# Kernel optimization log

Hardware: AMD Instinct MI355X
Metric: run time of the kernel (lower is better)

The kernel has to match this reference:

```python
import jax, jax.numpy as jnp
import numpy as np
import math

HEADS = 32
DIM_HEAD = 64
DM = HEADS * DIM_HEAD  # 2048
B, S = 2, 1024
BITS = 3
N_LEVELS = 2 ** BITS
N_GROUPS = (DIM_HEAD + 2) // 3  # 22
PAD = (3 - DIM_HEAD % 3) % 3    # 2
EPS_NORM = 1e-8
EPS_RMS = 1e-6


def _rotors_to_matrices(r):
    # r: (G,4) unit rotors [s, b12, b13, b23] -> (G,3,3) rotation matrices
    s, p, q, rr = r[:, 0], r[:, 1], r[:, 2], r[:, 3]
    s2, p2, q2, r2 = s * s, p * p, q * q, rr * rr
    M = np.zeros((r.shape[0], 3, 3), dtype=np.float32)
    M[:, 0, 0] = s2 - p2 - q2 + r2
    M[:, 0, 1] = 2 * s * p - 2 * q * rr
    M[:, 0, 2] = 2 * s * q + 2 * p * rr
    M[:, 1, 0] = -2 * s * p - 2 * q * rr
    M[:, 1, 1] = s2 - p2 + q2 - r2
    M[:, 1, 2] = 2 * s * rr - 2 * p * q
    M[:, 2, 0] = -2 * s * q + 2 * p * rr
    M[:, 2, 1] = -2 * s * rr - 2 * p * q
    M[:, 2, 2] = s2 + p2 - q2 - r2
    return M


def _make_compressor(seed):
    rng = np.random.default_rng(seed)
    rot = rng.standard_normal((N_GROUPS, 4)).astype(np.float32)
    rot /= np.linalg.norm(rot, axis=-1, keepdims=True)
    M = _rotors_to_matrices(rot)
    sigma = 1.0 / math.sqrt(DIM_HEAD)  # Lloyd-Max for N(0, 1/d)
    C = np.linspace(-3 * sigma, 3 * sigma, N_LEVELS, dtype=np.float32)
    return jnp.asarray(M), jnp.asarray(np.ascontiguousarray(M.transpose(0, 2, 1))), jnp.asarray(C)


def setup_inputs() -> dict:
    key = jax.random.key(0)
    ks = jax.random.split(key, 8)
    x = jax.random.normal(ks[0], (B, S, DM), dtype=jnp.float32)
    w_scale = 0.02
    Wq = jax.random.normal(ks[1], (DM, DM), dtype=jnp.float32) * w_scale
    Wk = jax.random.normal(ks[2], (DM, DM), dtype=jnp.float32) * w_scale
    Wv = jax.random.normal(ks[3], (DM, DM), dtype=jnp.float32) * w_scale
    Wo = jax.random.normal(ks[4], (DM, DM), dtype=jnp.float32) * w_scale
    qn_w = jnp.ones((DM,), dtype=jnp.float32)
    kn_w = jnp.ones((DM,), dtype=jnp.float32)
    Mk, Mtk, Ck = _make_compressor(42)
    Mv, Mtv, Cv = _make_compressor(4200)
    return {"x": x, "Wq": Wq, "Wk": Wk, "Wv": Wv, "Wo": Wo,
            "qn_w": qn_w, "kn_w": kn_w,
            "Mk": Mk, "Mtk": Mtk, "Ck": Ck,
            "Mv": Mv, "Mtv": Mtv, "Cv": Cv}


def _rmsnorm(x, w):
    return x * jax.lax.rsqrt(jnp.mean(x * x, axis=-1, keepdims=True) + EPS_RMS) * w


def _quant_roundtrip(h, M, Mt, C):
    """RotorQuant compress+decompress. h: (B,H,S,Dh) -> (B,H,S,Dh)."""
    norms = jnp.maximum(jnp.linalg.norm(h, axis=-1, keepdims=True), EPS_NORM)
    xu = h / norms
    xu = jnp.pad(xu, ((0, 0), (0, 0), (0, 0), (0, PAD)))
    g = xu.reshape(h.shape[0], h.shape[1], h.shape[2], N_GROUPS, 3)
    rot = jnp.einsum('bhsgi,gij->bhsgj', g, M)
    flat = rot.reshape(h.shape[0], h.shape[1], h.shape[2], N_GROUPS * 3)
    # nearest-centroid quantization (uint8 indices in original)
    idx = jnp.argmin(jnp.abs(flat[..., None] - C), axis=-1)
    deq = C[idx]
    g2 = deq.reshape(h.shape[0], h.shape[1], h.shape[2], N_GROUPS, 3)
    der = jnp.einsum('bhsgi,gij->bhsgj', g2, Mt)
    out = der.reshape(h.shape[0], h.shape[1], h.shape[2], N_GROUPS * 3)[..., :DIM_HEAD]
    return out * norms


def reference(x, Wq, Wk, Wv, Wo, qn_w, kn_w, Mk, Mtk, Ck, Mv, Mtv, Cv):
    b, s, _ = x.shape
    v = x @ Wv
    q = _rmsnorm(x @ Wq, qn_w)
    k = _rmsnorm(x @ Wk, kn_w)
    # split heads -> (B,H,S,Dh)
    qh = q.reshape(b, s, HEADS, DIM_HEAD).transpose(0, 2, 1, 3)
    kh = k.reshape(b, s, HEADS, DIM_HEAD).transpose(0, 2, 1, 3)
    vh = v.reshape(b, s, HEADS, DIM_HEAD).transpose(0, 2, 1, 3)
    # per-head rotor quantization roundtrip of K and V
    kh = _quant_roundtrip(kh, Mk, Mtk, Ck)
    vh = _quant_roundtrip(vh, Mv, Mtv, Cv)
    # scaled dot-product attention
    scores = jnp.einsum('bhqd,bhkd->bhqk', qh, kh) / math.sqrt(DIM_HEAD)
    probs = jax.nn.softmax(scores, axis=-1)
    o = jnp.einsum('bhqk,bhkd->bhqd', probs, vh)
    o = o.transpose(0, 2, 1, 3).reshape(b, s, DM)
    return o @ Wo
```

## Files before the change

kernel.cpp:

```cpp
#include <hip/hip_runtime.h>
#include <hip/hip_bf16.h>
#include <math.h>

#define HEADS 32
#define DIM_HEAD 64
#define DM 2048
#define BATCH 2
#define SEQ 1024
#define NROWS (BATCH * SEQ)
#define NVEC (NROWS * HEADS)
#define N_GROUPS 22
#define N_LEVELS 8
#define EPS_NORM 1e-8f
#define EPS_RMS 1e-6f

typedef float f32x4 __attribute__((ext_vector_type(4)));
typedef __bf16 bf16x8 __attribute__((ext_vector_type(8)));
typedef unsigned short u16x8 __attribute__((ext_vector_type(8)));
typedef unsigned short u16x4 __attribute__((ext_vector_type(4)));

__device__ __forceinline__ unsigned short f2bf(float x) {
  union { float f; unsigned u; } v; v.f = x;
  unsigned r = v.u + 0x7fffu + ((v.u >> 16) & 1u);
  return (unsigned short)(r >> 16);
}
__device__ __forceinline__ float bf2f(unsigned short h) {
  union { unsigned u; float f; } v; v.u = ((unsigned)h) << 16;
  return v.f;
}
__device__ __forceinline__ bf16x8 ldfrag(const unsigned short* p) {
  return __builtin_bit_cast(bf16x8, *(const u16x8*)p);
}
#define MFMA16(a, b, c) __builtin_amdgcn_mfma_f32_16x16x32_bf16((a), (b), (c), 0, 0, 0)

__device__ __forceinline__ void stage16(const unsigned short* g, unsigned short* lds) {
  __builtin_amdgcn_global_load_lds(
      (const __attribute__((address_space(1))) unsigned int*)g,
      (__attribute__((address_space(3))) unsigned int*)lds, 16, 0, 0);
}

#define WAITV(N) asm volatile("s_waitcnt vmcnt(" #N ")" ::: "memory")
#define WAITL0() asm volatile("s_waitcnt lgkmcnt(0)" ::: "memory")
#define SBARM()  asm volatile("s_barrier" ::: "memory")
#define SFENCE() __builtin_amdgcn_sched_barrier(0)

__global__ __launch_bounds__(256) void split_convert_kernel(
    const float* __restrict__ X, unsigned short* __restrict__ hi,
    unsigned short* __restrict__ lo, int n8) {
  const int i = blockIdx.x * 256 + threadIdx.x;
  if (i >= n8) return;
  const float4 a = ((const float4*)X)[2 * i];
  const float4 b = ((const float4*)X)[2 * i + 1];
  const float v[8] = {a.x, a.y, a.z, a.w, b.x, b.y, b.z, b.w};
  u16x8 h, l;
#pragma unroll
  for (int j = 0; j < 8; ++j) {
    const unsigned short hh = f2bf(v[j]);
    h[j] = hh;
    l[j] = f2bf(v[j] - bf2f(hh));
  }
  ((u16x8*)hi)[i] = h;
  if (lo) ((u16x8*)lo)[i] = l;
}

__global__ __launch_bounds__(256) void transpose_split_batch_kernel(
    const float* __restrict__ W0, const float* __restrict__ W1,
    const float* __restrict__ W2, const float* __restrict__ W3,
    unsigned short* __restrict__ T0h, unsigned short* __restrict__ T1h,
    unsigned short* __restrict__ T1l, unsigned short* __restrict__ T2h,
    unsigned short* __restrict__ T2l, unsigned short* __restrict__ T3h) {
  const int z = blockIdx.z;
  const float* W = (z == 0) ? W0 : (z == 1) ? W1 : (z == 2) ? W2 : W3;
  unsigned short* Th = (z == 0) ? T0h : (z == 1) ? T1h : (z == 2) ? T2h : T3h;
  unsigned short* Tl = (z == 1) ? T1l : (z == 2) ? T2l : nullptr;

  __shared__ float S[64][65];
  const int t = threadIdx.x;
  const int tk = blockIdx.y * 64, tm = blockIdx.x * 64;
  {
    const int r = t >> 2, cs = (t & 3) * 16;
    const float* src = W + (size_t)(tk + r) * DM + tm + cs;
#pragma unroll
    for (int j = 0; j < 16; j += 4) {
      float4 v = *(const float4*)(src + j);
      S[r][cs + j] = v.x; S[r][cs + j + 1] = v.y;
      S[r][cs + j + 2] = v.z; S[r][cs + j + 3] = v.w;
    }
  }
  __syncthreads();
  const int m = t >> 2, ks = (t & 3) * 16;
  u16x8 h0, h1, l0, l1;
#pragma unroll
  for (int j = 0; j < 8; ++j) {
    const float v = S[ks + j][m];
    const unsigned short hh = f2bf(v);
    h0[j] = hh; l0[j] = f2bf(v - bf2f(hh));
  }
#pragma unroll
  for (int j = 0; j < 8; ++j) {
    const float v = S[ks + 8 + j][m];
    const unsigned short hh = f2bf(v);
    h1[j] = hh; l1[j] = f2bf(v - bf2f(hh));
  }
  const size_t o = (size_t)(tm + m) * DM + tk + ks;
  *(u16x8*)&Th[o] = h0; *(u16x8*)&Th[o + 8] = h1;
  if (Tl) { *(u16x8*)&Tl[o] = l0; *(u16x8*)&Tl[o + 8] = l1; }
}

__global__ __launch_bounds__(512, 2) void gemm_plain8(
    const unsigned short* __restrict__ A, const unsigned short* __restrict__ B,
    float* __restrict__ C, int ntiles) {
  __shared__ unsigned short L[2][2][128 * 64];
  const int t = threadIdx.x, lane = t & 63, w = t >> 6;
  const int wr = w >> 2, wc = w & 3;
  const int gm0 = blockIdx.y * 128;
  const int gn0 = blockIdx.x * 128;
  const int z = blockIdx.z;
  const int k0 = z * (ntiles << 6);
  const int chunk = (lane & 7) ^ (lane >> 3);

  auto stg = [&](const unsigned short* g, int row0, int kt, unsigned short* dst) {
#pragma unroll
    for (int it = 0; it < 2; ++it) {
      const int r = (w << 4) + (it << 3) + (lane >> 3);
      stage16(g + (size_t)(row0 + r) * DM + kt + chunk * 8,
              dst + ((w << 4) + (it << 3)) * 64);
    }
  };

  f32x4 acc[4][2] = {};

  stg(A, gm0, k0, L[0][0]);
  stg(B, gn0, k0, L[0][1]);

  for (int tt = 0; tt < ntiles; ++tt) {
    const int c = tt & 1, n = c ^ 1;
    const bool pf = (tt + 1 < ntiles);
    if (pf) {
      const int ktn = k0 + ((tt + 1) << 6);
      stg(A, gm0, ktn, L[n][0]);
      stg(B, gn0, ktn, L[n][1]);
      WAITV(4);
    } else {
      WAITV(0);
    }
    SBARM(); SFENCE();
    const unsigned short* cA = L[c][0];
    const unsigned short* cB = L[c][1];
    bf16x8 fa[4][2], fb[2][2];
#pragma unroll
    for (int ks = 0; ks < 2; ++ks) {
      const int ch = ks * 4 + (lane >> 4);
#pragma unroll
      for (int i = 0; i < 4; ++i) {
        const int row = wr * 64 + i * 16 + (lane & 15);
        fa[i][ks] = ldfrag(&cA[row * 64 + ((ch ^ (row & 7)) << 3)]);
      }
#pragma unroll
      for (int j = 0; j < 2; ++j) {
        const int row = wc * 32 + j * 16 + (lane & 15);
        fb[j][ks] = ldfrag(&cB[row * 64 + ((ch ^ (row & 7)) << 3)]);
      }
    }
    WAITL0();
    __builtin_amdgcn_s_setprio(1);
#pragma unroll
    for (int i = 0; i < 4; ++i)
#pragma unroll
      for (int j = 0; j < 2; ++j)
#pragma unroll
        for (int ks = 0; ks < 2; ++ks)
          acc[i][j] = MFMA16(fa[i][ks], fb[j][ks], acc[i][j]);
    __builtin_amdgcn_s_setprio(0);
    SFENCE(); SBARM();
  }

  float* Cz = C + (size_t)z * NROWS * DM;
#pragma unroll
  for (int i = 0; i < 4; ++i) {
    const int row = gm0 + wr * 64 + i * 16 + ((lane >> 4) << 2);
#pragma unroll
    for (int j = 0; j < 2; ++j) {
      const int col = gn0 + wc * 32 + j * 16 + (lane & 15);
#pragma unroll
      for (int r = 0; r < 4; ++r)
        Cz[(size_t)(row + r) * DM + col] = acc[i][j][r];
    }
  }
}

__global__ __launch_bounds__(512, 2) void gemm_kv_split8(
    const unsigned short* __restrict__ Ah, const unsigned short* __restrict__ Al,
    const unsigned short* __restrict__ Bh, const unsigned short* __restrict__ Bl,
    float* __restrict__ kout, float* __restrict__ vout) {
  __shared__ unsigned short L[2][4][128 * 64];
  const int t = threadIdx.x, lane = t & 63, w = t >> 6;
  const int wr = w >> 2, wc = w & 3;
  const int gm0 = blockIdx.y * 128;
  const int nAbs = 2048 + blockIdx.x * 128;
  const int seg = nAbs >> 11;
  const int gn0 = nAbs & 2047;
  const int chunk = (lane & 7) ^ (lane >> 3);

  auto stg = [&](const unsigned short* g, int row0, int kt, unsigned short* dst) {
#pragma unroll
    for (int it = 0; it < 2; ++it) {
      const int r = (w << 4) + (it << 3) + (lane >> 3);
      stage16(g + (size_t)(row0 + r) * DM + kt + chunk * 8,
              dst + ((w << 4) + (it << 3)) * 64);
    }
  };

  f32x4 acc[4][2] = {};

  auto group = [&](const unsigned short* arrA, const unsigned short* arrB) {
    bf16x8 fa[4][2], fb[2][2];
#pragma unroll
    for (int ks = 0; ks < 2; ++ks) {
      const int ch = ks * 4 + (lane >> 4);
#pragma unroll
      for (int i = 0; i < 4; ++i) {
        const int row = wr * 64 + i * 16 + (lane & 15);
        fa[i][ks] = ldfrag(&arrA[row * 64 + ((ch ^ (row & 7)) << 3)]);
      }
#pragma unroll
      for (int j = 0; j < 2; ++j) {
        const int row = wc * 32 + j * 16 + (lane & 15);
        fb[j][ks] = ldfrag(&arrB[row * 64 + ((ch ^ (row & 7)) << 3)]);
      }
    }
    WAITL0();
    __builtin_amdgcn_s_setprio(1);
#pragma unroll
    for (int i = 0; i < 4; ++i)
#pragma unroll
      for (int j = 0; j < 2; ++j)
#pragma unroll
        for (int ks = 0; ks < 2; ++ks)
          acc[i][j] = MFMA16(fa[i][ks], fb[j][ks], acc[i][j]);
    __builtin_amdgcn_s_setprio(0);
  };

  stg(Ah, gm0, 0, L[0][0]);
  stg(Bh, nAbs, 0, L[0][1]);
  stg(Bl, nAbs, 0, L[0][2]);
  stg(Al, gm0, 0, L[0][3]);

  for (int tt = 0; tt < 32; ++tt) {
    const int c = tt & 1, n = c ^ 1;
    const bool pf = (tt + 1 < 32);
    const int ktn = (tt + 1) << 6;

    if (pf) { stg(Ah, gm0, ktn, L[n][0]); stg(Bh, nAbs, ktn, L[n][1]); WAITV(8); }
    else WAITV(4);
    SBARM(); SFENCE();
    group(L[c][0], L[c][1]);
    SFENCE(); SBARM();

    if (pf) { stg(Bl, nAbs, ktn, L[n][2]); WAITV(8); }
    else WAITV(2);
    SBARM(); SFENCE();
    group(L[c][0], L[c][2]);
    SFENCE(); SBARM();

    if (pf) { stg(Al, gm0, ktn, L[n][3]); WAITV(8); }
    else WAITV(0);
    SBARM(); SFENCE();
    group(L[c][3], L[c][1]);
    SFENCE(); SBARM();
  }

  float* C = (seg == 1) ? kout : vout;
#pragma unroll
  for (int i = 0; i < 4; ++i) {
    const int row = gm0 + wr * 64 + i * 16 + ((lane >> 4) << 2);
#pragma unroll
    for (int j = 0; j < 2; ++j) {
      const int col = gn0 + wc * 32 + j * 16 + (lane & 15);
#pragma unroll
      for (int r = 0; r < 4; ++r)
        C[(size_t)(row + r) * DM + col] = acc[i][j][r];
    }
  }
}

__global__ __launch_bounds__(256) void add2_f4_kernel(
    const float* __restrict__ a, const float* __restrict__ b,
    float* __restrict__ o, int n4) {
  const int i = blockIdx.x * 256 + threadIdx.x;
  if (i >= n4) return;
  const float4 x = ((const float4*)a)[i];
  const float4 y = ((const float4*)b)[i];
  ((float4*)o)[i] = make_float4(x.x + y.x, x.y + y.y, x.z + y.z, x.w + y.w);
}

__device__ __forceinline__ float wave_sum(float x) {
#pragma unroll
  for (int o = 32; o > 0; o >>= 1) x += __shfl_xor(x, o, 64);
  return x;
}

__global__ __launch_bounds__(256) void rmsnorm_kernel(
    float* __restrict__ y, const float* __restrict__ w) {
  __shared__ float rbuf[4];
  const int row = blockIdx.x;
  float* p = y + (size_t)row * DM;
  const int t = threadIdx.x;
  const int wave = t >> 6, lane = t & 63;

  float ss = 0.f;
#pragma unroll
  for (int c = t; c < DM; c += 256) { float v = p[c]; ss += v * v; }
  ss = wave_sum(ss);
  if (lane == 0) rbuf[wave] = ss;
  __syncthreads();
  ss = rbuf[0] + rbuf[1] + rbuf[2] + rbuf[3];
  const float scale = rsqrtf(ss * (1.0f / DM) + EPS_RMS);
#pragma unroll
  for (int c = t; c < DM; c += 256) p[c] = p[c] * scale * w[c];
}

__global__ __launch_bounds__(256) void rmsnorm_split_kernel(
    const float* __restrict__ y, const float* __restrict__ w,
    unsigned short* __restrict__ hi, unsigned short* __restrict__ lo,
    float post) {
  __shared__ float rbuf[4];
  const int row = blockIdx.x;
  const float* p = y + (size_t)row * DM;
  const int t = threadIdx.x;
  const int wave = t >> 6, lane = t & 63;

  const int c0 = t * 8;
  float4 a = *(const float4*)(p + c0);
  float4 b = *(const float4*)(p + c0 + 4);
  float v[8] = {a.x, a.y, a.z, a.w, b.x, b.y, b.z, b.w};
  float ss = 0.f;
#pragma unroll
  for (int j = 0; j < 8; ++j) ss += v[j] * v[j];
  ss = wave_sum(ss);
  if (lane == 0) rbuf[wave] = ss;
  __syncthreads();
  ss = rbuf[0] + rbuf[1] + rbuf[2] + rbuf[3];
  const float scale = rsqrtf(ss * (1.0f / DM) + EPS_RMS) * post;

  u16x8 hv, lv;
#pragma unroll
  for (int j = 0; j < 8; ++j) {
    const float val = v[j] * scale * w[c0 + j];
    const unsigned short hh = f2bf(val);
    hv[j] = hh; lv[j] = f2bf(val - bf2f(hh));
  }
  *(u16x8*)&hi[(size_t)row * DM + c0] = hv;
  *(u16x8*)&lo[(size_t)row * DM + c0] = lv;
}

__device__ __forceinline__ float qnearest(float v, const float* __restrict__ C) {
  float best = C[0];
  float bd = fabsf(v - C[0]);
#pragma unroll
  for (int i = 1; i < N_LEVELS; ++i) {
    float d = fabsf(v - C[i]);
    if (d < bd) { bd = d; best = C[i]; }
  }
  return best;
}

template <bool WRITE_BF>
__global__ __launch_bounds__(256) void quant_kernel(
    float* __restrict__ kv, const float* __restrict__ M,
    const float* __restrict__ Mt, const float* __restrict__ C,
    unsigned short* __restrict__ hi, unsigned short* __restrict__ lo) {
  const int vec = blockIdx.x * blockDim.x + threadIdx.x;
  if (vec >= NVEC) return;
  float* p = kv + (size_t)vec * DIM_HEAD;

  float h[66];
  float ss = 0.f;
#pragma unroll
  for (int d = 0; d < DIM_HEAD; ++d) { h[d] = p[d]; ss += h[d] * h[d]; }
  float norm = fmaxf(sqrtf(ss), EPS_NORM);
  const float inv = 1.0f / norm;
#pragma unroll
  for (int d = 0; d < DIM_HEAD; ++d) h[d] *= inv;
  h[64] = 0.f; h[65] = 0.f;

#pragma unroll
  for (int g = 0; g < N_GROUPS; ++g) {
    const float* Mg  = M  + g * 9;
    const float* Mtg = Mt + g * 9;
    const float a0 = h[3 * g + 0], a1 = h[3 * g + 1], a2 = h[3 * g + 2];
    const float r0 = a0 * Mg[0] + a1 * Mg[3] + a2 * Mg[6];
    const float r1 = a0 * Mg[1] + a1 * Mg[4] + a2 * Mg[7];
    const float r2 = a0 * Mg[2] + a1 * Mg[5] + a2 * Mg[8];
    const float d0 = qnearest(r0, C);
    const float d1 = qnearest(r1, C);
    const float d2 = qnearest(r2, C);
    h[3 * g + 0] = d0 * Mtg[0] + d1 * Mtg[3] + d2 * Mtg[6];
    h[3 * g + 1] = d0 * Mtg[1] + d1 * Mtg[4] + d2 * Mtg[7];
    h[3 * g + 2] = d0 * Mtg[2] + d1 * Mtg[5] + d2 * Mtg[8];
  }
  if (WRITE_BF) {
#pragma unroll
    for (int g8 = 0; g8 < 8; ++g8) {
      u16x8 hv, lv;
#pragma unroll
      for (int j = 0; j < 8; ++j) {
        const float val = h[g8 * 8 + j] * norm;
        const unsigned short hh = f2bf(val);
        hv[j] = hh; lv[j] = f2bf(val - bf2f(hh));
      }
      *(u16x8*)&hi[(size_t)vec * DIM_HEAD + g8 * 8] = hv;
      *(u16x8*)&lo[(size_t)vec * DIM_HEAD + g8 * 8] = lv;
    }
  } else {
#pragma unroll
    for (int d = 0; d < DIM_HEAD; ++d) p[d] = h[d] * norm;
  }
}

__global__ __launch_bounds__(256) void vt_split_kernel(
    const float* __restrict__ v, unsigned short* __restrict__ hi,
    unsigned short* __restrict__ lo) {
  __shared__ float T[64][65];
  const int s0 = blockIdx.x * 64;
  const int bh = blockIdx.y;
  const int b = bh >> 5, h = bh & 31;
  const int t = threadIdx.x;
  {
    const int sr = t >> 2, dseg = (t & 3) * 16;
    const float* src = v + ((size_t)(b * SEQ + s0 + sr) * DM + h * 64 + dseg);
#pragma unroll
    for (int j = 0; j < 16; j += 4) {
      float4 a = *(const float4*)(src + j);
      T[sr][dseg + j] = a.x; T[sr][dseg + j + 1] = a.y;
      T[sr][dseg + j + 2] = a.z; T[sr][dseg + j + 3] = a.w;
    }
  }
  __syncthreads();
  const int d = t >> 2, sseg = (t & 3) * 16;
  u16x8 h0, h1, l0, l1;
#pragma unroll
  for (int j = 0; j < 8; ++j) {
    const float val = T[sseg + j][d];
    const unsigned short hh = f2bf(val);
    h0[j] = hh; l0[j] = f2bf(val - bf2f(hh));
  }
#pragma unroll
  for (int j = 0; j < 8; ++j) {
    const float val = T[sseg + 8 + j][d];
    const unsigned short hh = f2bf(val);
    h1[j] = hh; l1[j] = f2bf(val - bf2f(hh));
  }
  const size_t o = (size_t)(bh * 64 + d) * SEQ + s0 + sseg;
  *(u16x8*)&hi[o] = h0; *(u16x8*)&hi[o + 8] = h1;
  *(u16x8*)&lo[o] = l0; *(u16x8*)&lo[o + 8] = l1;
}

__global__ __launch_bounds__(256) void attn_mfma_kernel(
    const unsigned short* __restrict__ qhi, const unsigned short* __restrict__ qlo,
    const unsigned short* __restrict__ khi, const unsigned short* __restrict__ klo,
    const unsigned short* __restrict__ vthi, const unsigned short* __restrict__ vtlo,
    unsigned short* __restrict__ ohi) {
  __shared__ unsigned short Ks_h[4096], Ks_l[4096];
  __shared__ unsigned short Vt_h[4096], Vt_l[4096];
  __shared__ unsigned int   Ps[4096];

  const int bh = blockIdx.x;
  const int qt = blockIdx.y;
  const int h = bh & 31, b = bh >> 5;
  const int q0 = qt * 64;
  const int t = threadIdx.x, lane = t & 63, w = t >> 6;
  const int quad = lane >> 4, l15 = lane & 15;
  const int srow = lane >> 3, schunk = lane & 7;

  auto stage = [&](const unsigned short* g, int stride, unsigned short* arr) {
#pragma unroll
    for (int it = 0; it < 2; ++it) {
      const int r = w * 16 + it * 8 + srow;
      const int c = schunk ^ (r & 7);
      stage16(g + (size_t)r * stride + c * 8, arr + (w * 16 + it * 8) * 64);
    }
  };

  bf16x8 qh[2], ql[2];
  {
    const size_t qrow = (size_t)(b * SEQ + q0 + w * 16 + l15) * DM + h * 64;
#pragma unroll
    for (int ks = 0; ks < 2; ++ks) {
      qh[ks] = ldfrag(&qhi[qrow + ks * 32 + quad * 8]);
      ql[ks] = ldfrag(&qlo[qrow + ks * 32 + quad * 8]);
    }
  }

  f32x4 acc[4] = {};
  float m_prev[4] = {-INFINITY, -INFINITY, -INFINITY, -INFINITY};
  float lsum[4] = {0.f, 0.f, 0.f, 0.f};

  const unsigned short* gkh = khi + ((size_t)(b * SEQ) * DM + h * 64);
  const unsigned short* gkl = klo + ((size_t)(b * SEQ) * DM + h * 64);
  const unsigned short* gvh = vthi + (size_t)(bh * 64) * SEQ;
  const unsigned short* gvl = vtlo + (size_t)(bh * 64) * SEQ;

  for (int kt = 0; kt < SEQ; kt += 64) {
    __syncthreads();
    stage(gkh + (size_t)kt * DM, DM, Ks_h);
    stage(gkl + (size_t)kt * DM, DM, Ks_l);
    stage(gvh + kt, SEQ, Vt_h);
    stage(gvl + kt, SEQ, Vt_l);
    __syncthreads();

    f32x4 s[4] = {};
#pragma unroll
    for (int nt = 0; nt < 4; ++nt) {
#pragma unroll
      for (int ks = 0; ks < 2; ++ks) {
        const int row = nt * 16 + l15;
        const int off = row * 64 + (((quad + 4 * ks) ^ (row & 7)) << 3);
        const bf16x8 kh = ldfrag(&Ks_h[off]);
        const bf16x8 kl = ldfrag(&Ks_l[off]);
        s[nt] = MFMA16(qh[ks], kh, s[nt]);
        s[nt] = MFMA16(qh[ks], kl, s[nt]);
        s[nt] = MFMA16(ql[ks], kh, s[nt]);
      }
    }

    float asave[4];
#pragma unroll
    for (int r = 0; r < 4; ++r) {
      float mx = fmaxf(fmaxf(s[0][r], s[1][r]), fmaxf(s[2][r], s[3][r]));
#pragma unroll
      for (int off = 1; off < 16; off <<= 1) mx = fmaxf(mx, __shfl_xor(mx, off, 64));
      const float mn = fmaxf(m_prev[r], mx);
      const float al = __expf(m_prev[r] - mn);
      float rs = 0.f;
#pragma unroll
      for (int nt = 0; nt < 4; ++nt) {
        const float e = __expf(s[nt][r] - mn);
        s[nt][r] = e; rs += e;
      }
#pragma unroll
      for (int off = 1; off < 16; off <<= 1) rs += __shfl_xor(rs, off, 64);
      lsum[r] = lsum[r] * al + rs;
      m_prev[r] = mn;
      asave[r] = al;
      const int prow = w * 16 + quad * 4 + r;
#pragma unroll
      for (int nt = 0; nt < 4; ++nt) {
        const int kk = nt * 16 + l15;
        const unsigned short hh = f2bf(s[nt][r]);
        const unsigned short ll = f2bf(s[nt][r] - bf2f(hh));
        Ps[prow * 64 + (kk ^ ((prow & 7) << 3))] =
            ((unsigned)hh << 16) | (unsigned)ll;
      }
    }

    {
      const int src = (l15 >> 2) << 4;
      const float a0 = __shfl(asave[0], src, 64);
      const float a1 = __shfl(asave[1], src, 64);
      const float a2 = __shfl(asave[2], src, 64);
      const float a3 = __shfl(asave[3], src, 64);
      const int rr = l15 & 3;
      const float alph = (rr == 0) ? a0 : (rr == 1) ? a1 : (rr == 2) ? a2 : a3;
#pragma unroll
      for (int mt = 0; mt < 4; ++mt) acc[mt] *= alph;
    }

    bf16x8 ph[2], pl[2];
#pragma unroll
    for (int ks = 0; ks < 2; ++ks) {
      const int prow = w * 16 + l15;
      const unsigned int* pp =
          &Ps[prow * 64 + ((ks * 32 + quad * 8) ^ ((prow & 7) << 3))];
      const uint4 pa = *(const uint4*)pp;
      const uint4 pb = *(const uint4*)(pp + 4);
      u16x8 hv, lv;
      const unsigned int pw[8] = {pa.x, pa.y, pa.z, pa.w, pb.x, pb.y, pb.z, pb.w};
#pragma unroll
      for (int j = 0; j < 8; ++j) {
        hv[j] = (unsigned short)(pw[j] >> 16);
        lv[j] = (unsigned short)(pw[j] & 0xffffu);
      }
      ph[ks] = __builtin_bit_cast(bf16x8, hv);
      pl[ks] = __builtin_bit_cast(bf16x8, lv);
    }

#pragma unroll
    for (int mt = 0; mt < 4; ++mt) {
#pragma unroll
      for (int ks = 0; ks < 2; ++ks) {
        const int drow = mt * 16 + l15;
        const int offv = drow * 64 + (((quad + 4 * ks) ^ (drow & 7)) << 3);
        const bf16x8 vh = ldfrag(&Vt_h[offv]);
        const bf16x8 vl = ldfrag(&Vt_l[offv]);
        acc[mt] = MFMA16(vh, ph[ks], acc[mt]);
        acc[mt] = MFMA16(vh, pl[ks], acc[mt]);
        acc[mt] = MFMA16(vl, ph[ks], acc[mt]);
      }
    }
  }

  {
    const int src = (l15 >> 2) << 4;
    const float a0 = __shfl(lsum[0], src, 64);
    const float a1 = __shfl(lsum[1], src, 64);
    const float a2 = __shfl(lsum[2], src, 64);
    const float a3 = __shfl(lsum[3], src, 64);
    const int rr = l15 & 3;
    const float lq = (rr == 0) ? a0 : (rr == 1) ? a1 : (rr == 2) ? a2 : a3;
    const float inv = 1.0f / lq;
    const size_t obase = (size_t)(b * SEQ + q0 + w * 16 + l15) * DM + h * 64;
#pragma unroll
    for (int mt = 0; mt < 4; ++mt) {
      u16x4 ov;
#pragma unroll
      for (int r = 0; r < 4; ++r) ov[r] = f2bf(acc[mt][r] * inv);
      *(u16x4*)&ohi[obase + mt * 16 + quad * 4] = ov;
    }
  }
}

extern "C" void kernel_launch(void* const* d_in, const int* in_sizes, int n_in,
                              void* d_out, int out_size, void* d_ws, size_t ws_size,
                              hipStream_t stream) {
  const float* x    = (const float*)d_in[0];
  const float* Wq   = (const float*)d_in[1];
  const float* Wk   = (const float*)d_in[2];
  const float* Wv   = (const float*)d_in[3];
  const float* Wo   = (const float*)d_in[4];
  const float* qn_w = (const float*)d_in[5];
  const float* kn_w = (const float*)d_in[6];
  const float* Mk   = (const float*)d_in[7];
  const float* Mtk  = (const float*)d_in[8];
  const float* Ck   = (const float*)d_in[9];
  const float* Mv   = (const float*)d_in[10];
  const float* Mtv  = (const float*)d_in[11];
  const float* Cv   = (const float*)d_in[12];
  float* out = (float*)d_out;

  const size_t MBb = 1024ull * 1024ull;
  const size_t SEG = (size_t)DM * DM;
  char* w = (char*)d_ws;
  float* qb = (float*)(w + 0 * MBb);
  float* kb = (float*)(w + 16 * MBb);
  float* vb = (float*)(w + 32 * MBb);
  unsigned short* xhi     = (unsigned short*)(w + 48 * MBb);
  unsigned short* xlo     = (unsigned short*)(w + 56 * MBb);
  unsigned short* wcat_hi = (unsigned short*)(w + 64 * MBb);
  unsigned short* wcat_lo = (unsigned short*)(w + 88 * MBb);
  unsigned short* wot     = (unsigned short*)(w + 112 * MBb);
  unsigned short* q_hi  = wcat_hi;
  unsigned short* k_hi  = wcat_hi + SEG;
  unsigned short* k_lo  = wcat_hi + 2 * SEG;
  unsigned short* q_lo  = wcat_lo;
  unsigned short* vt_hi = wcat_lo + SEG;
  unsigned short* vt_lo = wcat_lo + 2 * SEG;
  unsigned short* o_hi  = xhi;
  float* opart = (float*)(w + 0 * MBb);

  const int n8 = (NROWS * DM) / 8;

  split_convert_kernel<<<n8 / 256, 256, 0, stream>>>(x, xhi, xlo, n8);
  transpose_split_batch_kernel<<<dim3(DM / 64, DM / 64, 4), 256, 0, stream>>>(
      Wq, Wk, Wv, Wo,
      wcat_hi, wcat_hi + SEG, wcat_lo + SEG, wcat_hi + 2 * SEG, wcat_lo + 2 * SEG, wot);

  gemm_plain8<<<dim3(DM / 128, NROWS / 128, 1), 512, 0, stream>>>(
      xhi, wcat_hi, qb, DM / 64);
  gemm_kv_split8<<<dim3(2 * DM / 128, NROWS / 128), 512, 0, stream>>>(
      xhi, xlo, wcat_hi, wcat_lo, kb, vb);

  rmsnorm_kernel<<<NROWS, 256, 0, stream>>>(kb, kn_w);
  rmsnorm_split_kernel<<<NROWS, 256, 0, stream>>>(qb, qn_w, q_hi, q_lo, 0.125f);

  quant_kernel<true ><<<NVEC / 256, 256, 0, stream>>>(kb, Mk, Mtk, Ck, k_hi, k_lo);
  quant_kernel<false><<<NVEC / 256, 256, 0, stream>>>(vb, Mv, Mtv, Cv, nullptr, nullptr);
  vt_split_kernel<<<dim3(SEQ / 64, BATCH * HEADS), 256, 0, stream>>>(vb, vt_hi, vt_lo);

  attn_mfma_kernel<<<dim3(BATCH * HEADS, SEQ / 64), 256, 0, stream>>>(
      q_hi, q_lo, k_hi, k_lo, vt_hi, vt_lo, o_hi);

  gemm_plain8<<<dim3(DM / 128, NROWS / 128, 2), 512, 0, stream>>>(
      o_hi, wot, opart, DM / 64 / 2);
  add2_f4_kernel<<<(NROWS * DM / 4 + 255) / 256, 256, 0, stream>>>(
      opart, opart + (size_t)NROWS * DM, out, NROWS * DM / 4);
}
```

Before: 481.9 us.

## Use 256x256 GEMM tiles with split-K and fuse partial sums into consumers

```diff
diff --git a/kernel.cpp b/kernel.cpp
--- a/kernel.cpp
+++ b/kernel.cpp
@@ -40,7 +40,6 @@
 }
 
 #define WAITV(N) asm volatile("s_waitcnt vmcnt(" #N ")" ::: "memory")
-#define WAITL0() asm volatile("s_waitcnt lgkmcnt(0)" ::: "memory")
 #define SBARM()  asm volatile("s_barrier" ::: "memory")
 #define SFENCE() __builtin_amdgcn_sched_barrier(0)
 
@@ -107,28 +106,133 @@
   if (Tl) { *(u16x8*)&Tl[o] = l0; *(u16x8*)&Tl[o + 8] = l1; }
 }
 
-__global__ __launch_bounds__(512, 2) void gemm_plain8(
-    const unsigned short* __restrict__ A, const unsigned short* __restrict__ B,
-    float* __restrict__ C, int ntiles) {
-  __shared__ unsigned short L[2][2][128 * 64];
+
+__global__ __launch_bounds__(512, 2) void gemm_kv3_kernel(
+    const unsigned short* __restrict__ Ah, const unsigned short* __restrict__ Al,
+    const unsigned short* __restrict__ Bh, const unsigned short* __restrict__ Bl,
+    float* __restrict__ kout, float* __restrict__ vout,
+    float* __restrict__ kpart, float* __restrict__ vpart, int ntiles) {
+  __shared__ unsigned short L[2][4][256 * 32];
+
   const int t = threadIdx.x, lane = t & 63, w = t >> 6;
   const int wr = w >> 2, wc = w & 3;
-  const int gm0 = blockIdx.y * 128;
-  const int gn0 = blockIdx.x * 128;
-  const int z = blockIdx.z;
-  const int k0 = z * (ntiles << 6);
-  const int chunk = (lane & 7) ^ (lane >> 3);
+  const int gm0 = blockIdx.y * 256;
+  const int x = blockIdx.x;
+  const int seg = x >> 3;
+  const int gn0 = (x & 7) * 256;
+  const int nAbs = 2048 + x * 256;
+  const int k0 = blockIdx.z * (ntiles << 5);
+  const int quad = lane >> 4, l15 = lane & 15;
+  const int srow = lane >> 2, schunk = lane & 3;
 
   auto stg = [&](const unsigned short* g, int row0, int kt, unsigned short* dst) {
 #pragma unroll
     for (int it = 0; it < 2; ++it) {
-      const int r = (w << 4) + (it << 3) + (lane >> 3);
-      stage16(g + (size_t)(row0 + r) * DM + kt + chunk * 8,
-              dst + ((w << 4) + (it << 3)) * 64);
+      const int r = (w << 5) + (it << 4) + srow;
+      const int cg = schunk ^ (r & 3);
+      stage16(g + (size_t)(row0 + r) * DM + kt + cg * 8,
+              dst + (((w << 5) + (it << 4)) << 5));
     }
   };
 
-  f32x4 acc[4][2] = {};
+  f32x4 acc[8][4] = {};
+  bf16x8 fa[8], fb[4];
+
+  auto rdA = [&](const unsigned short* arr) {
+#pragma unroll
+    for (int i = 0; i < 8; ++i) {
+      const int row = wr * 128 + i * 16 + l15;
+      fa[i] = ldfrag(&arr[row * 32 + ((quad ^ (row & 3)) << 3)]);
+    }
+  };
+  auto rdB = [&](const unsigned short* arr) {
+#pragma unroll
+    for (int j = 0; j < 4; ++j) {
+      const int row = wc * 64 + j * 16 + l15;
+      fb[j] = ldfrag(&arr[row * 32 + ((quad ^ (row & 3)) << 3)]);
+    }
+  };
+  auto mm = [&]() {
+    __builtin_amdgcn_s_setprio(1);
+#pragma unroll
+    for (int i = 0; i < 8; ++i)
+#pragma unroll
+      for (int j = 0; j < 4; ++j)
+        acc[i][j] = MFMA16(fa[i], fb[j], acc[i][j]);
+    __builtin_amdgcn_s_setprio(0);
+  };
+
+  stg(Ah, gm0, k0, L[0][0]);
+  stg(Bh, nAbs, k0, L[0][1]);
+  stg(Bl, nAbs, k0, L[0][2]);
+  stg(Al, gm0, k0, L[0][3]);
+
+  for (int tt = 0; tt < ntiles; ++tt) {
+    const int c = tt & 1, n = c ^ 1;
+    const bool pf = (tt + 1 < ntiles);
+    const int ktn = k0 + ((tt + 1) << 5);
+
+    if (pf) { stg(Ah, gm0, ktn, L[n][0]); stg(Bh, nAbs, ktn, L[n][1]); WAITV(8); }
+    else WAITV(4);
+    SBARM(); SFENCE();
+    rdA(L[c][0]); rdB(L[c][1]);
+    mm();
+    SFENCE(); SBARM();
+
+    if (pf) { stg(Bl, nAbs, ktn, L[n][2]); WAITV(8); }
+    else WAITV(2);
+    SBARM(); SFENCE();
+    rdB(L[c][2]);
+    mm();
+    SFENCE(); SBARM();
+
+    if (pf) { stg(Al, gm0, ktn, L[n][3]); WAITV(8); }
+    else WAITV(0);
+    SBARM(); SFENCE();
+    rdA(L[c][3]); rdB(L[c][1]);
+    mm();
+    SFENCE(); SBARM();
+  }
+
+  float* C = (blockIdx.z == 0) ? (seg ? vout : kout) : (seg ? vpart : kpart);
+#pragma unroll
+  for (int i = 0; i < 8; ++i) {
+    const int row = gm0 + wr * 128 + i * 16 + quad * 4;
+#pragma unroll
+    for (int j = 0; j < 4; ++j) {
+      const int col = gn0 + wc * 64 + j * 16 + l15;
+#pragma unroll
+      for (int r = 0; r < 4; ++r)
+        C[(size_t)(row + r) * DM + col] = acc[i][j][r];
+    }
+  }
+}
+
+__global__ __launch_bounds__(512, 2) void gemm_plain256_kernel(
+    const unsigned short* __restrict__ A, const unsigned short* __restrict__ B,
+    float* __restrict__ C0, float* __restrict__ Cpart, int ntiles) {
+  __shared__ unsigned short L[2][2][256 * 32];
+
+  const int t = threadIdx.x, lane = t & 63, w = t >> 6;
+  const int wr = w >> 2, wc = w & 3;
+  const int gm0 = blockIdx.y * 256;
+  const int gn0 = blockIdx.x * 256;
+  const int k0 = blockIdx.z * (ntiles << 5);
+  const int quad = lane >> 4, l15 = lane & 15;
+  const int srow = lane >> 2, schunk = lane & 3;
+
+  auto stg = [&](const unsigned short* g, int row0, int kt, unsigned short* dst) {
+#pragma unroll
+    for (int it = 0; it < 2; ++it) {
+      const int r = (w << 5) + (it << 4) + srow;
+      const int cg = schunk ^ (r & 3);
+      stage16(g + (size_t)(row0 + r) * DM + kt + cg * 8,
+              dst + (((w << 5) + (it << 4)) << 5));
+    }
+  };
+
+  f32x4 acc[8][4] = {};
+  bf16x8 fa[8], fb[4];
 
   stg(A, gm0, k0, L[0][0]);
   stg(B, gn0, k0, L[0][1]);
@@ -137,7 +241,7 @@
     const int c = tt & 1, n = c ^ 1;
     const bool pf = (tt + 1 < ntiles);
     if (pf) {
-      const int ktn = k0 + ((tt + 1) << 6);
+      const int ktn = k0 + ((tt + 1) << 5);
       stg(A, gm0, ktn, L[n][0]);
       stg(B, gn0, ktn, L[n][1]);
       WAITV(4);
@@ -145,138 +249,33 @@
       WAITV(0);
     }
     SBARM(); SFENCE();
-    const unsigned short* cA = L[c][0];
-    const unsigned short* cB = L[c][1];
-    bf16x8 fa[4][2], fb[2][2];
-#pragma unroll
-    for (int ks = 0; ks < 2; ++ks) {
-      const int ch = ks * 4 + (lane >> 4);
-#pragma unroll
-      for (int i = 0; i < 4; ++i) {
-        const int row = wr * 64 + i * 16 + (lane & 15);
-        fa[i][ks] = ldfrag(&cA[row * 64 + ((ch ^ (row & 7)) << 3)]);
-      }
-#pragma unroll
-      for (int j = 0; j < 2; ++j) {
-        const int row = wc * 32 + j * 16 + (lane & 15);
-        fb[j][ks] = ldfrag(&cB[row * 64 + ((ch ^ (row & 7)) << 3)]);
-      }
-    }
-    WAITL0();
+#pragma unroll
+    for (int i = 0; i < 8; ++i) {
+      const int row = wr * 128 + i * 16 + l15;
+      fa[i] = ldfrag(&L[c][0][row * 32 + ((quad ^ (row & 3)) << 3)]);
+    }
+#pragma unroll
+    for (int j = 0; j < 4; ++j) {
+      const int row = wc * 64 + j * 16 + l15;
+      fb[j] = ldfrag(&L[c][1][row * 32 + ((quad ^ (row & 3)) << 3)]);
+    }
     __builtin_amdgcn_s_setprio(1);
 #pragma unroll
-    for (int i = 0; i < 4; ++i)
-#pragma unroll
-      for (int j = 0; j < 2; ++j)
-#pragma unroll
-        for (int ks = 0; ks < 2; ++ks)
-          acc[i][j] = MFMA16(fa[i][ks], fb[j][ks], acc[i][j]);
+    for (int i = 0; i < 8; ++i)
+#pragma unroll
+      for (int j = 0; j < 4; ++j)
+        acc[i][j] = MFMA16(fa[i], fb[j], acc[i][j]);
     __builtin_amdgcn_s_setprio(0);
     SFENCE(); SBARM();
   }
 
-  float* Cz = C + (size_t)z * NROWS * DM;
-#pragma unroll
-  for (int i = 0; i < 4; ++i) {
-    const int row = gm0 + wr * 64 + i * 16 + ((lane >> 4) << 2);
-#pragma unroll
-    for (int j = 0; j < 2; ++j) {
-      const int col = gn0 + wc * 32 + j * 16 + (lane & 15);
-#pragma unroll
-      for (int r = 0; r < 4; ++r)
-        Cz[(size_t)(row + r) * DM + col] = acc[i][j][r];
-    }
-  }
-}
-
-__global__ __launch_bounds__(512, 2) void gemm_kv_split8(
-    const unsigned short* __restrict__ Ah, const unsigned short* __restrict__ Al,
-    const unsigned short* __restrict__ Bh, const unsigned short* __restrict__ Bl,
-    float* __restrict__ kout, float* __restrict__ vout) {
-  __shared__ unsigned short L[2][4][128 * 64];
-  const int t = threadIdx.x, lane = t & 63, w = t >> 6;
-  const int wr = w >> 2, wc = w & 3;
-  const int gm0 = blockIdx.y * 128;
-  const int nAbs = 2048 + blockIdx.x * 128;
-  const int seg = nAbs >> 11;
-  const int gn0 = nAbs & 2047;
-  const int chunk = (lane & 7) ^ (lane >> 3);
-
-  auto stg = [&](const unsigned short* g, int row0, int kt, unsigned short* dst) {
-#pragma unroll
-    for (int it = 0; it < 2; ++it) {
-      const int r = (w << 4) + (it << 3) + (lane >> 3);
-      stage16(g + (size_t)(row0 + r) * DM + kt + chunk * 8,
-              dst + ((w << 4) + (it << 3)) * 64);
-    }
-  };
-
-  f32x4 acc[4][2] = {};
-
-  auto group = [&](const unsigned short* arrA, const unsigned short* arrB) {
-    bf16x8 fa[4][2], fb[2][2];
-#pragma unroll
-    for (int ks = 0; ks < 2; ++ks) {
-      const int ch = ks * 4 + (lane >> 4);
-#pragma unroll
-      for (int i = 0; i < 4; ++i) {
-        const int row = wr * 64 + i * 16 + (lane & 15);
-        fa[i][ks] = ldfrag(&arrA[row * 64 + ((ch ^ (row & 7)) << 3)]);
-      }
-#pragma unroll
-      for (int j = 0; j < 2; ++j) {
-        const int row = wc * 32 + j * 16 + (lane & 15);
-        fb[j][ks] = ldfrag(&arrB[row * 64 + ((ch ^ (row & 7)) << 3)]);
-      }
-    }
-    WAITL0();
-    __builtin_amdgcn_s_setprio(1);
-#pragma unroll
-    for (int i = 0; i < 4; ++i)
-#pragma unroll
-      for (int j = 0; j < 2; ++j)
-#pragma unroll
-        for (int ks = 0; ks < 2; ++ks)
-          acc[i][j] = MFMA16(fa[i][ks], fb[j][ks], acc[i][j]);
-    __builtin_amdgcn_s_setprio(0);
-  };
-
-  stg(Ah, gm0, 0, L[0][0]);
-  stg(Bh, nAbs, 0, L[0][1]);
-  stg(Bl, nAbs, 0, L[0][2]);
-  stg(Al, gm0, 0, L[0][3]);
-
-  for (int tt = 0; tt < 32; ++tt) {
-    const int c = tt & 1, n = c ^ 1;
-    const bool pf = (tt + 1 < 32);
-    const int ktn = (tt + 1) << 6;
-
-    if (pf) { stg(Ah, gm0, ktn, L[n][0]); stg(Bh, nAbs, ktn, L[n][1]); WAITV(8); }
-    else WAITV(4);
-    SBARM(); SFENCE();
-    group(L[c][0], L[c][1]);
-    SFENCE(); SBARM();
-
-    if (pf) { stg(Bl, nAbs, ktn, L[n][2]); WAITV(8); }
-    else WAITV(2);
-    SBARM(); SFENCE();
-    group(L[c][0], L[c][2]);
-    SFENCE(); SBARM();
-
-    if (pf) { stg(Al, gm0, ktn, L[n][3]); WAITV(8); }
-    else WAITV(0);
-    SBARM(); SFENCE();
-    group(L[c][3], L[c][1]);
-    SFENCE(); SBARM();
-  }
-
-  float* C = (seg == 1) ? kout : vout;
-#pragma unroll
-  for (int i = 0; i < 4; ++i) {
-    const int row = gm0 + wr * 64 + i * 16 + ((lane >> 4) << 2);
-#pragma unroll
-    for (int j = 0; j < 2; ++j) {
-      const int col = gn0 + wc * 32 + j * 16 + (lane & 15);
+  float* C = (blockIdx.z == 0) ? C0 : (Cpart + (size_t)(blockIdx.z - 1) * NROWS * DM);
+#pragma unroll
+  for (int i = 0; i < 8; ++i) {
+    const int row = gm0 + wr * 128 + i * 16 + quad * 4;
+#pragma unroll
+    for (int j = 0; j < 4; ++j) {
+      const int col = gn0 + wc * 64 + j * 16 + l15;
 #pragma unroll
       for (int r = 0; r < 4; ++r)
         C[(size_t)(row + r) * DM + col] = acc[i][j][r];
@@ -284,14 +283,17 @@
   }
 }
 
-__global__ __launch_bounds__(256) void add2_f4_kernel(
-    const float* __restrict__ a, const float* __restrict__ b,
-    float* __restrict__ o, int n4) {
+__global__ __launch_bounds__(256) void add3_rmw_kernel(
+    float* __restrict__ o, const float* __restrict__ p0,
+    const float* __restrict__ p1, const float* __restrict__ p2, int n4) {
   const int i = blockIdx.x * 256 + threadIdx.x;
   if (i >= n4) return;
-  const float4 x = ((const float4*)a)[i];
-  const float4 y = ((const float4*)b)[i];
-  ((float4*)o)[i] = make_float4(x.x + y.x, x.y + y.y, x.z + y.z, x.w + y.w);
+  const float4 a = ((const float4*)o)[i];
+  const float4 x = ((const float4*)p0)[i];
+  const float4 y = ((const float4*)p1)[i];
+  const float4 z = ((const float4*)p2)[i];
+  ((float4*)o)[i] = make_float4(a.x + x.x + y.x + z.x, a.y + x.y + y.y + z.y,
+                                a.z + x.z + y.z + z.z, a.w + x.w + y.w + z.w);
 }
 
 __device__ __forceinline__ float wave_sum(float x) {
@@ -301,29 +303,46 @@
 }
 
 __global__ __launch_bounds__(256) void rmsnorm_kernel(
-    float* __restrict__ y, const float* __restrict__ w) {
+    float* __restrict__ y, const float* __restrict__ part,
+    const float* __restrict__ w) {
   __shared__ float rbuf[4];
   const int row = blockIdx.x;
   float* p = y + (size_t)row * DM;
   const int t = threadIdx.x;
   const int wave = t >> 6, lane = t & 63;
 
+  const int c0 = t * 8;
+  float4 a = *(const float4*)(p + c0);
+  float4 b = *(const float4*)(p + c0 + 4);
+  float v[8] = {a.x, a.y, a.z, a.w, b.x, b.y, b.z, b.w};
+  if (part) {
+    const float* pp = part + (size_t)row * DM + c0;
+    float4 pa = *(const float4*)pp;
+    float4 pb = *(const float4*)(pp + 4);
+    v[0] += pa.x; v[1] += pa.y; v[2] += pa.z; v[3] += pa.w;
+    v[4] += pb.x; v[5] += pb.y; v[6] += pb.z; v[7] += pb.w;
+  }
   float ss = 0.f;
 #pragma unroll
-  for (int c = t; c < DM; c += 256) { float v = p[c]; ss += v * v; }
+  for (int j = 0; j < 8; ++j) ss += v[j] * v[j];
   ss = wave_sum(ss);
   if (lane == 0) rbuf[wave] = ss;
   __syncthreads();
   ss = rbuf[0] + rbuf[1] + rbuf[2] + rbuf[3];
   const float scale = rsqrtf(ss * (1.0f / DM) + EPS_RMS);
-#pragma unroll
-  for (int c = t; c < DM; c += 256) p[c] = p[c] * scale * w[c];
+  float4 o0, o1;
+  o0.x = v[0] * scale * w[c0 + 0]; o0.y = v[1] * scale * w[c0 + 1];
+  o0.z = v[2] * scale * w[c0 + 2]; o0.w = v[3] * scale * w[c0 + 3];
+  o1.x = v[4] * scale * w[c0 + 4]; o1.y = v[5] * scale * w[c0 + 5];
+  o1.z = v[6] * scale * w[c0 + 6]; o1.w = v[7] * scale * w[c0 + 7];
+  *(float4*)(p + c0) = o0;
+  *(float4*)(p + c0 + 4) = o1;
 }
 
 __global__ __launch_bounds__(256) void rmsnorm_split_kernel(
-    const float* __restrict__ y, const float* __restrict__ w,
-    unsigned short* __restrict__ hi, unsigned short* __restrict__ lo,
-    float post) {
+    const float* __restrict__ y, const float* __restrict__ part,
+    const float* __restrict__ w, unsigned short* __restrict__ hi,
+    unsigned short* __restrict__ lo, float post) {
   __shared__ float rbuf[4];
   const int row = blockIdx.x;
   const float* p = y + (size_t)row * DM;
@@ -334,6 +353,13 @@
   float4 a = *(const float4*)(p + c0);
   float4 b = *(const float4*)(p + c0 + 4);
   float v[8] = {a.x, a.y, a.z, a.w, b.x, b.y, b.z, b.w};
+  if (part) {
+    const float* pp = part + (size_t)row * DM + c0;
+    float4 pa = *(const float4*)pp;
+    float4 pb = *(const float4*)(pp + 4);
+    v[0] += pa.x; v[1] += pa.y; v[2] += pa.z; v[3] += pa.w;
+    v[4] += pb.x; v[5] += pb.y; v[6] += pb.z; v[7] += pb.w;
+  }
   float ss = 0.f;
 #pragma unroll
   for (int j = 0; j < 8; ++j) ss += v[j] * v[j];
@@ -367,17 +393,25 @@
 
 template <bool WRITE_BF>
 __global__ __launch_bounds__(256) void quant_kernel(
-    float* __restrict__ kv, const float* __restrict__ M,
-    const float* __restrict__ Mt, const float* __restrict__ C,
-    unsigned short* __restrict__ hi, unsigned short* __restrict__ lo) {
+    float* __restrict__ kv, const float* __restrict__ part,
+    const float* __restrict__ M, const float* __restrict__ Mt,
+    const float* __restrict__ C, unsigned short* __restrict__ hi,
+    unsigned short* __restrict__ lo) {
   const int vec = blockIdx.x * blockDim.x + threadIdx.x;
   if (vec >= NVEC) return;
   float* p = kv + (size_t)vec * DIM_HEAD;
 
   float h[66];
+#pragma unroll
+  for (int d = 0; d < DIM_HEAD; ++d) h[d] = p[d];
+  if (part) {
+    const float* pp = part + (size_t)vec * DIM_HEAD;
+#pragma unroll
+    for (int d = 0; d < DIM_HEAD; ++d) h[d] += pp[d];
+  }
   float ss = 0.f;
 #pragma unroll
-  for (int d = 0; d < DIM_HEAD; ++d) { h[d] = p[d]; ss += h[d] * h[d]; }
+  for (int d = 0; d < DIM_HEAD; ++d) ss += h[d] * h[d];
   float norm = fmaxf(sqrtf(ss), EPS_NORM);
   const float inv = 1.0f / norm;
 #pragma unroll
@@ -649,6 +683,10 @@
   unsigned short* wcat_hi = (unsigned short*)(w + 64 * MBb);
   unsigned short* wcat_lo = (unsigned short*)(w + 88 * MBb);
   unsigned short* wot     = (unsigned short*)(w + 112 * MBb);
+  const bool big = ws_size >= 168ull * MBb;
+  float* kpart = big ? (float*)(w + 120 * MBb) : nullptr;
+  float* vpart = big ? (float*)(w + 136 * MBb) : nullptr;
+  float* qpart = big ? (float*)(w + 152 * MBb) : nullptr;
   unsigned short* q_hi  = wcat_hi;
   unsigned short* k_hi  = wcat_hi + SEG;
   unsigned short* k_lo  = wcat_hi + 2 * SEG;
@@ -656,32 +694,35 @@
   unsigned short* vt_hi = wcat_lo + SEG;
   unsigned short* vt_lo = wcat_lo + 2 * SEG;
   unsigned short* o_hi  = xhi;
-  float* opart = (float*)(w + 0 * MBb);
+  float* opart3 = (float*)(w + 64 * MBb);
 
   const int n8 = (NROWS * DM) / 8;
+  const int zkv = big ? 2 : 1;
+  const int zq  = big ? 2 : 1;
 
   split_convert_kernel<<<n8 / 256, 256, 0, stream>>>(x, xhi, xlo, n8);
   transpose_split_batch_kernel<<<dim3(DM / 64, DM / 64, 4), 256, 0, stream>>>(
       Wq, Wk, Wv, Wo,
       wcat_hi, wcat_hi + SEG, wcat_lo + SEG, wcat_hi + 2 * SEG, wcat_lo + 2 * SEG, wot);
 
-  gemm_plain8<<<dim3(DM / 128, NROWS / 128, 1), 512, 0, stream>>>(
-      xhi, wcat_hi, qb, DM / 64);
-  gemm_kv_split8<<<dim3(2 * DM / 128, NROWS / 128), 512, 0, stream>>>(
-      xhi, xlo, wcat_hi, wcat_lo, kb, vb);
-
-  rmsnorm_kernel<<<NROWS, 256, 0, stream>>>(kb, kn_w);
-  rmsnorm_split_kernel<<<NROWS, 256, 0, stream>>>(qb, qn_w, q_hi, q_lo, 0.125f);
-
-  quant_kernel<true ><<<NVEC / 256, 256, 0, stream>>>(kb, Mk, Mtk, Ck, k_hi, k_lo);
-  quant_kernel<false><<<NVEC / 256, 256, 0, stream>>>(vb, Mv, Mtv, Cv, nullptr, nullptr);
+  gemm_kv3_kernel<<<dim3(16, 8, zkv), 512, 0, stream>>>(
+      xhi, xlo, wcat_hi, wcat_lo, kb, vb, kpart, vpart, 64 / zkv);
+  gemm_plain256_kernel<<<dim3(8, 8, zq), 512, 0, stream>>>(
+      xhi, wcat_hi, qb, qpart, 64 / zq);
+
+  rmsnorm_kernel<<<NROWS, 256, 0, stream>>>(kb, kpart, kn_w);
+  rmsnorm_split_kernel<<<NROWS, 256, 0, stream>>>(qb, qpart, qn_w, q_hi, q_lo, 0.125f);
+
+  quant_kernel<true ><<<NVEC / 256, 256, 0, stream>>>(kb, nullptr, Mk, Mtk, Ck, k_hi, k_lo);
+  quant_kernel<false><<<NVEC / 256, 256, 0, stream>>>(vb, vpart, Mv, Mtv, Cv, nullptr, nullptr);
   vt_split_kernel<<<dim3(SEQ / 64, BATCH * HEADS), 256, 0, stream>>>(vb, vt_hi, vt_lo);
 
   attn_mfma_kernel<<<dim3(BATCH * HEADS, SEQ / 64), 256, 0, stream>>>(
       q_hi, q_lo, k_hi, k_lo, vt_hi, vt_lo, o_hi);
 
-  gemm_plain8<<<dim3(DM / 128, NROWS / 128, 2), 512, 0, stream>>>(
-      o_hi, wot, opart, DM / 64 / 2);
-  add2_f4_kernel<<<(NROWS * DM / 4 + 255) / 256, 256, 0, stream>>>(
-      opart, opart + (size_t)NROWS * DM, out, NROWS * DM / 4);
-}
+  gemm_plain256_kernel<<<dim3(8, 8, 4), 512, 0, stream>>>(
+      o_hi, wot, out, opart3, 16);
+  add3_rmw_kernel<<<(NROWS * DM / 4 + 255) / 256, 256, 0, stream>>>(
+      out, opart3, opart3 + (size_t)NROWS * DM, opart3 + 2 * (size_t)NROWS * DM,
+      NROWS * DM / 4);
+}
```

New measurement: 516.2 us. 7.1% more time.
